# Optimization experiments

Measured on AMD Instinct MI355X. Metric: run time of the kernel, lower is better.

## Reference

```python
import jax, jax.numpy as jnp
import numpy as np

EPS = 1e-5
B, D_ENT, D_REL = 1024, 400, 400
OUT, KW = 32, 9
N_ENT = 50000


def _bn(x, g, b, axes):
    # batch-norm with batch statistics (training-mode math), eps=1e-5
    mu = jnp.mean(x, axis=axes, keepdims=True)
    var = jnp.var(x, axis=axes, keepdims=True)
    return (x - mu) * jax.lax.rsqrt(var + EPS) * g + b


def setup_inputs() -> dict:
    key = jax.random.key(0)
    ks = jax.random.split(key, 6)
    return {
        "e1_emb": jax.random.normal(ks[0], (B, D_ENT), jnp.float32),
        "rel_emb": jax.random.normal(ks[1], (B, D_REL), jnp.float32),
        "all_ent_w": jax.random.normal(ks[2], (N_ENT, D_ENT), jnp.float32),
        "fc1_w": jax.random.normal(ks[3], (OUT * KW, D_REL), jnp.float32) * 0.05,
        "fc1_b": jnp.zeros((OUT * KW,), jnp.float32),
        "fc_w": jax.random.normal(ks[4], (D_ENT, (D_ENT - KW + 1) * OUT), jnp.float32) * 0.02,
        "fc_b": jnp.zeros((D_ENT,), jnp.float32),
        "bn0_g": jnp.ones((1,), jnp.float32),
        "bn0_b": jnp.zeros((1,), jnp.float32),
        "bn1_g": jnp.ones((OUT,), jnp.float32),
        "bn1_b": jnp.zeros((OUT,), jnp.float32),
        "bn2_g": jnp.ones((D_ENT,), jnp.float32),
        "bn2_b": jnp.zeros((D_ENT,), jnp.float32),
    }


def reference(e1_emb, rel_emb, all_ent_w, fc1_w, fc1_b, fc_w, fc_b,
              bn0_g, bn0_b, bn1_g, bn1_b, bn2_g, bn2_b):
    d = e1_emb.shape[1]
    L = d - KW + 1  # conv output width (kernel_h=1, in_channels=1)

    # bn0: BatchNorm2d(1) over view [B,1,1,d] -> stats over all elements
    x = _bn(e1_emb, bn0_g, bn0_b, axes=(0, 1))  # [B, d]

    # hypernetwork: relation -> per-sample conv kernels [B, OUT, KW]
    k = (rel_emb @ fc1_w.T + fc1_b).reshape(-1, OUT, KW)

    # per-sample 1x9 conv (groups=B) as windows + batched contraction
    # xw[b, l, w] = x[b, l + w]
    xw = jnp.stack([x[:, w:w + L] for w in range(KW)], axis=-1)  # [B, L, KW]
    conv = jnp.einsum('blw,bow->bol', xw, k)  # [B, OUT, L]

    # bn1: BatchNorm2d(OUT), per-channel stats over (batch, width)
    h = _bn(conv, bn1_g[None, :, None], bn1_b[None, :, None], axes=(0, 2))

    # flatten channel-major (matches torch .view(B, -1) on [B, OUT, 1, L])
    h = h.reshape(h.shape[0], OUT * L)
    h = h @ fc_w.T + fc_b  # [B, d]

    # bn2: BatchNorm1d(d), per-feature stats over batch
    h = jax.nn.relu(_bn(h, bn2_g, bn2_b, axes=(0,)))

    return h @ all_ent_w.T  # [B, N_ENT]
```

## Files before the change

kernel.cpp:

```cpp
#include <hip/hip_runtime.h>
#include <stdint.h>

typedef unsigned short u16;
typedef short bf16x8 __attribute__((ext_vector_type(8)));
typedef float f32x4 __attribute__((ext_vector_type(4)));
typedef u16 u16x4 __attribute__((ext_vector_type(4)));
typedef u16 u16x8 __attribute__((ext_vector_type(8)));

#define B_SZ   1024
#define D_IN   400
#define L_OUT  392
#define OC     32
#define KW     9
#define K_FC   12544
#define N_ENT  50000
#define KPAD_H 448
#define NPAD_FC 512
#define SPLIT_FC 14

__device__ __forceinline__ u16 f2bf(float f) {
  uint32_t u = __builtin_bit_cast(uint32_t, f);
  u += 0x7FFFu + ((u >> 16) & 1u);
  return (u16)(u >> 16);
}
__device__ __forceinline__ float bf2f(u16 v) {
  uint32_t u = ((uint32_t)v) << 16;
  return __builtin_bit_cast(float, u);
}

__device__ __forceinline__ void gload_lds16(const u16* g, u16* l) {
  __builtin_amdgcn_global_load_lds(
      (const __attribute__((address_space(1))) unsigned int*)g,
      (__attribute__((address_space(3))) unsigned int*)l, 16, 0, 0);
}

__device__ __forceinline__ void block_reduce2(float& s1, float& s2, float* sm) {
  for (int d = 32; d; d >>= 1) { s1 += __shfl_down(s1, d); s2 += __shfl_down(s2, d); }
  int wave = threadIdx.x >> 6, lane = threadIdx.x & 63;
  if (lane == 0) { sm[wave * 2] = s1; sm[wave * 2 + 1] = s2; }
  __syncthreads();
  if (threadIdx.x == 0) {
    s1 = sm[0] + sm[2] + sm[4] + sm[6];
    s2 = sm[1] + sm[3] + sm[5] + sm[7];
  }
}

__global__ __launch_bounds__(256) void red0(const float* __restrict__ e1, float* __restrict__ part0) {
  int t = threadIdx.x;
  int idx = blockIdx.x * 256 + t;
  float s1 = 0.f, s2 = 0.f;
  for (int i = idx; i < B_SZ * D_IN; i += 256 * 256) { float v = e1[i]; s1 += v; s2 += v * v; }
  __shared__ float sm[8];
  block_reduce2(s1, s2, sm);
  if (t == 0) { part0[blockIdx.x * 2] = s1; part0[blockIdx.x * 2 + 1] = s2; }
}

__global__ __launch_bounds__(256) void fc1_gemm(const float* __restrict__ rel,
                                                const float* __restrict__ W,
                                                const float* __restrict__ bias,
                                                float* __restrict__ outk,
                                                const float* __restrict__ part0,
                                                const float* __restrict__ g0,
                                                const float* __restrict__ b0,
                                                float* __restrict__ stats) {
  __shared__ __align__(16) float As[16 * 68];
  __shared__ __align__(16) float Bs[16 * 68];
  __shared__ float sm0[8];
  int mt = blockIdx.x, nt = blockIdx.y;
  int t = threadIdx.x;
  int tx = t & 15, ty = t >> 4;
  int lr = t >> 2, lk = (t & 3) * 4;
  float acc[4][4] = {};
  for (int k0 = 0; k0 < 400; k0 += 16) {
    __syncthreads();
    float4 av = *(const float4*)(rel + (size_t)(mt * 64 + lr) * 400 + k0 + lk);
    int brow = nt * 64 + lr;
    float4 bv = {0.f, 0.f, 0.f, 0.f};
    if (brow < 288) bv = *(const float4*)(W + (size_t)brow * 400 + k0 + lk);
    As[(lk + 0) * 68 + lr] = av.x; As[(lk + 1) * 68 + lr] = av.y;
    As[(lk + 2) * 68 + lr] = av.z; As[(lk + 3) * 68 + lr] = av.w;
    Bs[(lk + 0) * 68 + lr] = bv.x; Bs[(lk + 1) * 68 + lr] = bv.y;
    Bs[(lk + 2) * 68 + lr] = bv.z; Bs[(lk + 3) * 68 + lr] = bv.w;
    __syncthreads();
#pragma unroll
    for (int k = 0; k < 16; ++k) {
      float4 a = *(const float4*)(As + k * 68 + ty * 4);
      float4 b = *(const float4*)(Bs + k * 68 + tx * 4);
      float aa[4] = {a.x, a.y, a.z, a.w}, bb[4] = {b.x, b.y, b.z, b.w};
#pragma unroll
      for (int i = 0; i < 4; ++i)
#pragma unroll
        for (int j = 0; j < 4; ++j) acc[i][j] += aa[i] * bb[j];
    }
  }
#pragma unroll
  for (int i = 0; i < 4; ++i) {
    int row = mt * 64 + ty * 4 + i;
#pragma unroll
    for (int j = 0; j < 4; ++j) {
      int col = nt * 64 + tx * 4 + j;
      if (col < 288) outk[(size_t)row * 288 + col] = acc[i][j] + bias[col];
    }
  }
  if (mt == 0 && nt == 0) {
    float s1 = part0[t * 2], s2 = part0[t * 2 + 1];
    __syncthreads();
    block_reduce2(s1, s2, sm0);
    if (t == 0) {
      const float N = (float)(B_SZ * D_IN);
      float mu = s1 / N, var = s2 / N - mu * mu;
      float a = g0[0] * rsqrtf(var + 1e-5f);
      stats[0] = a;
      stats[1] = b0[0] - mu * a;
    }
  }
}

__global__ __launch_bounds__(256) void conv_kernel(const float* __restrict__ e1,
                                                   const float* __restrict__ stats,
                                                   const float* __restrict__ kbuf,
                                                   u16* __restrict__ convA,
                                                   float* __restrict__ partial1) {
  int b = blockIdx.x, t = threadIdx.x;
  __shared__ __align__(16) float xs[D_IN];
  __shared__ float ks[OC * KW];
  float a0 = stats[0], b0c = stats[1];
  for (int i = t; i < D_IN; i += 256) xs[i] = e1[(size_t)b * D_IN + i] * a0 + b0c;
  for (int i = t; i < OC * KW; i += 256) ks[i] = kbuf[(size_t)b * (OC * KW) + i];
  __syncthreads();
  int o = t >> 3, sub = t & 7;
  float kw[KW];
#pragma unroll
  for (int w = 0; w < KW; ++w) kw[w] = ks[o * KW + w];
  float s1 = 0.f, s2 = 0.f;
  u16* orow = convA + (size_t)b * K_FC + o * L_OUT;
#pragma unroll
  for (int it = 0; it < 13; ++it) {
    int l = sub * 4 + it * 32;
    if (l < L_OUT) {
      float4 x0 = *(const float4*)(xs + l);
      float4 x1 = *(const float4*)(xs + l + 4);
      float4 x2 = *(const float4*)(xs + l + 8);
      float xv[12] = {x0.x, x0.y, x0.z, x0.w, x1.x, x1.y, x1.z, x1.w, x2.x, x2.y, x2.z, x2.w};
      u16x4 st;
#pragma unroll
      for (int j = 0; j < 4; ++j) {
        float c = 0.f;
#pragma unroll
        for (int w = 0; w < KW; ++w) c += xv[j + w] * kw[w];
        s1 += c; s2 += c * c;
        st[j] = f2bf(c);
      }
      *(u16x4*)(orow + l) = st;
    }
  }
  s1 += __shfl_down(s1, 4); s2 += __shfl_down(s2, 4);
  s1 += __shfl_down(s1, 2); s2 += __shfl_down(s2, 2);
  s1 += __shfl_down(s1, 1); s2 += __shfl_down(s2, 1);
  if (sub == 0) {
    partial1[b * 64 + o] = s1;
    partial1[b * 64 + 32 + o] = s2;
  }
}

__global__ __launch_bounds__(256) void comb1(const float* __restrict__ partial1,
                                             const float* __restrict__ g1,
                                             float* __restrict__ alphaK) {
  __shared__ float red[256];
  __shared__ float ab[32];
  int t = threadIdx.x;
  int s = t & 63, q = t >> 6;
  float acc = 0.f;
  for (int b = q * 256; b < q * 256 + 256; ++b) acc += partial1[b * 64 + s];
  red[t] = acc;
  __syncthreads();
  if (t < 64) red[t] = red[t] + red[t + 64] + red[t + 128] + red[t + 192];
  __syncthreads();
  if (t < 32) {
    const float N = (float)(B_SZ * L_OUT);
    float S1 = red[t], S2 = red[t + 32];
    float mu = S1 / N, var = S2 / N - mu * mu;
    ab[t] = g1[t] * rsqrtf(var + 1e-5f);
  }
  __syncthreads();
  for (int i = t; i < K_FC; i += 256) {
    int o = i / L_OUT;
    alphaK[i] = ab[o];
  }
}

__global__ __launch_bounds__(256) void cvt_fcw(const float* __restrict__ src,
                                               const float* __restrict__ alphaK,
                                               u16* __restrict__ dst) {
  int gid = blockIdx.x * 256 + threadIdx.x;
  int row = gid / 1568, c = gid - row * 1568;
  int k = c * 8;
  u16x8 o = {};
  if (row < 400) {
    float4 f0 = *(const float4*)(src + (size_t)row * K_FC + k);
    float4 f1 = *(const float4*)(src + (size_t)row * K_FC + k + 4);
    float4 a0 = *(const float4*)(alphaK + k);
    float4 a1 = *(const float4*)(alphaK + k + 4);
    o[0] = f2bf(f0.x * a0.x); o[1] = f2bf(f0.y * a0.y);
    o[2] = f2bf(f0.z * a0.z); o[3] = f2bf(f0.w * a0.w);
    o[4] = f2bf(f1.x * a1.x); o[5] = f2bf(f1.y * a1.y);
    o[6] = f2bf(f1.z * a1.z); o[7] = f2bf(f1.w * a1.w);
  }
  *(u16x8*)(dst + (size_t)row * K_FC + k) = o;
}

__global__ __launch_bounds__(256) void bn2_kernel(const float* __restrict__ part2,
                                                  const float* __restrict__ g2,
                                                  const float* __restrict__ b2,
                                                  u16* __restrict__ hfin) {
  int j0 = blockIdx.x * 16;
  int t = threadIdx.x;
  int tj = t & 15, tb = t >> 4;
  int j = j0 + tj;
  float v[64];
  float s1 = 0.f, s2 = 0.f;
#pragma unroll 2
  for (int i = 0; i < 64; ++i) {
    int b = tb + i * 16;
    float acc = 0.f;
#pragma unroll
    for (int s = 0; s < SPLIT_FC; ++s)
      acc += part2[((size_t)s * B_SZ + b) * NPAD_FC + j];
    v[i] = acc; s1 += acc; s2 += acc * acc;
  }
  __shared__ float sm1[16][17], sm2[16][17];
  sm1[tb][tj] = s1; sm2[tb][tj] = s2;
  __syncthreads();
  __shared__ float albe[2][16];
  if (t < 16) {
    float S1 = 0.f, S2 = 0.f;
#pragma unroll
    for (int r = 0; r < 16; ++r) { S1 += sm1[r][t]; S2 += sm2[r][t]; }
    int jf = j0 + t;
    float al = 0.f, be = 0.f;
    if (jf < D_IN) {
      float mu = S1 / 1024.f, var = S2 / 1024.f - mu * mu;
      al = g2[jf] * rsqrtf(var + 1e-5f);
      be = b2[jf] - mu * al;
    }
    albe[0][t] = al; albe[1][t] = be;
  }
  __syncthreads();
  float al = albe[0][tj], be = albe[1][tj];
#pragma unroll 2
  for (int i = 0; i < 64; ++i) {
    int b = tb + i * 16;
    hfin[(size_t)b * KPAD_H + j] = f2bf(fmaxf(v[i] * al + be, 0.f));
  }
}

__global__ __launch_bounds__(256) void gemm_bt(const u16* __restrict__ A,
                                               const u16* __restrict__ Bm,
                                               float* __restrict__ C,
                                               int Kpad, int mtiles, int ntiles,
                                               int ksteps_total, int ksteps_chunk,
                                               long ldc, int ncols_valid, long csplit_stride) {
  __shared__ __align__(16) u16 As[128 * 64];
  __shared__ __align__(16) u16 Bs[128 * 64];
  int bid = blockIdx.x;
  int mt = bid % mtiles;
  int nt = (bid / mtiles) % ntiles;
  int sp = bid / (mtiles * ntiles);
  int kbeg = sp * ksteps_chunk;
  int kend = kbeg + ksteps_chunk;
  if (kend > ksteps_total) kend = ksteps_total;

  int tid = threadIdx.x;
  int wave = tid >> 6, lane = tid & 63;
  int quad = lane >> 4, m16 = lane & 15;
  int rbase = (wave >> 1) * 64, cbase = (wave & 1) * 64;

  const u16* Arow0 = A + (size_t)mt * 128 * Kpad;
  const u16* Brow0 = Bm + (size_t)nt * 128 * Kpad;

  f32x4 acc[4][4] = {};

  for (int kt = kbeg; kt < kend; ++kt) {
    int k0 = kt * 64;
    __syncthreads();
#pragma unroll
    for (int p = 0; p < 4; ++p) {
      int slin = p * 256 + tid;
      int row = slin >> 3;
      int gch = (slin & 7) ^ (row & 7);
      u16* la = As + ((p * 256 + (wave << 6)) << 3);
      u16* lb = Bs + ((p * 256 + (wave << 6)) << 3);
      gload_lds16(Arow0 + (size_t)row * Kpad + k0 + gch * 8, la);
      gload_lds16(Brow0 + (size_t)row * Kpad + k0 + gch * 8, lb);
    }
    __syncthreads();
#pragma unroll
    for (int s = 0; s < 2; ++s) {
      bf16x8 af[4], bfr[4];
#pragma unroll
      for (int i = 0; i < 4; ++i) {
        int ar = rbase + i * 16 + m16;
        af[i] = *(const bf16x8*)(As + ar * 64 + (((s * 4 + quad) ^ (ar & 7)) << 3));
        int bc = cbase + i * 16 + m16;
        bfr[i] = *(const bf16x8*)(Bs + bc * 64 + (((s * 4 + quad) ^ (bc & 7)) << 3));
      }
#pragma unroll
      for (int i = 0; i < 4; ++i)
#pragma unroll
        for (int j = 0; j < 4; ++j)
          acc[i][j] = __builtin_amdgcn_mfma_f32_16x16x32_bf16(af[i], bfr[j], acc[i][j], 0, 0, 0);
    }
  }

  float* Cb = C + (size_t)sp * csplit_stride;
#pragma unroll
  for (int i = 0; i < 4; ++i) {
#pragma unroll
    for (int j = 0; j < 4; ++j) {
      int col = nt * 128 + cbase + j * 16 + m16;
      if (col < ncols_valid) {
        int row0 = mt * 128 + rbase + i * 16 + quad * 4;
#pragma unroll
        for (int r = 0; r < 4; ++r)
          Cb[(size_t)(row0 + r) * ldc + col] = acc[i][j][r];
      }
    }
  }
}

__global__ __launch_bounds__(256, 2) void gemm_ent(const u16* __restrict__ A,
                                                   const float* __restrict__ Bf,
                                                   float* __restrict__ C) {
  __shared__ __align__(16) u16 As[2][256 * 64];
  __shared__ __align__(16) u16 Bs[128 * 64];
  int bid = blockIdx.x;
  int r = bid & 7, g = bid >> 3;
  int mt = g & 3;
  int nt = (g >> 2) * 8 + r;
  if (nt >= 391) return;

  int tid = threadIdx.x;
  int wave = tid >> 6, lane = tid & 63;
  int quad = lane >> 4, m16 = lane & 15;
  int rbase = (wave >> 1) * 128, cbase = (wave & 1) * 64;

  const u16* Arow0 = A + (size_t)mt * 256 * KPAD_H;

  float4 fb[4][2];

#define LOAD_B(K0)                                                         \
  {                                                                        \
    _Pragma("unroll") for (int q = 0; q < 4; ++q) {                        \
      int slin = q * 256 + tid;                                            \
      int row = slin >> 3;                                                 \
      int gch = (slin & 7) ^ (row & 7);                                    \
      int gr = nt * 128 + row;                                             \
      int gk = (K0) + gch * 8;                                             \
      if (gr < N_ENT && gk < D_IN) {                                       \
        fb[q][0] = *(const float4*)(Bf + (size_t)gr * D_IN + gk);          \
        fb[q][1] = *(const float4*)(Bf + (size_t)gr * D_IN + gk + 4);      \
      } else {                                                             \
        fb[q][0] = float4{0.f, 0.f, 0.f, 0.f};                             \
        fb[q][1] = float4{0.f, 0.f, 0.f, 0.f};                             \
      }                                                                    \
    }                                                                      \
  }

#define STAGE_A(KT, BUF)                                                   \
  {                                                                        \
    _Pragma("unroll") for (int p = 0; p < 8; ++p) {                        \
      int slin = p * 256 + tid;                                            \
      int row = slin >> 3;                                                 \
      int gch = (slin & 7) ^ (row & 7);                                    \
      u16* la = As[BUF] + ((p * 256 + (wave << 6)) << 3);                  \
      gload_lds16(Arow0 + (size_t)row * KPAD_H + (KT) * 64 + gch * 8, la); \
    }                                                                      \
  }

#define WRITE_B()                                                          \
  {                                                                        \
    _Pragma("unroll") for (int q = 0; q < 4; ++q) {                        \
      int slin = q * 256 + tid;                                            \
      u16x8 st;                                                            \
      st[0] = f2bf(fb[q][0].x); st[1] = f2bf(fb[q][0].y);                  \
      st[2] = f2bf(fb[q][0].z); st[3] = f2bf(fb[q][0].w);                  \
      st[4] = f2bf(fb[q][1].x); st[5] = f2bf(fb[q][1].y);                  \
      st[6] = f2bf(fb[q][1].z); st[7] = f2bf(fb[q][1].w);                  \
      *(u16x8*)(Bs + slin * 8) = st;                                       \
    }                                                                      \
  }

  f32x4 acc[8][4] = {};

  LOAD_B(0)
  STAGE_A(0, 0)

#pragma unroll
  for (int kt = 0; kt < 7; ++kt) {
    int cur = kt & 1;
    WRITE_B()
    if (kt < 6) {
      LOAD_B((kt + 1) * 64)
      STAGE_A(kt + 1, cur ^ 1)
    }
    __builtin_amdgcn_sched_barrier(0);
    if (kt < 6) asm volatile("s_waitcnt vmcnt(16) lgkmcnt(0)" ::: "memory");
    else        asm volatile("s_waitcnt vmcnt(0) lgkmcnt(0)" ::: "memory");
    __builtin_amdgcn_sched_barrier(0);
    __builtin_amdgcn_s_barrier();
    __builtin_amdgcn_sched_barrier(0);

    __builtin_amdgcn_s_setprio(1);
#pragma unroll
    for (int s = 0; s < 2; ++s) {
      bf16x8 bfr[4];
#pragma unroll
      for (int j = 0; j < 4; ++j) {
        int bc = cbase + j * 16 + m16;
        bfr[j] = *(const bf16x8*)(Bs + bc * 64 + (((s * 4 + quad) ^ (bc & 7)) << 3));
      }
#pragma unroll
      for (int i = 0; i < 8; ++i) {
        int ar = rbase + i * 16 + m16;
        bf16x8 af = *(const bf16x8*)(As[cur] + ar * 64 + (((s * 4 + quad) ^ (ar & 7)) << 3));
#pragma unroll
        for (int j = 0; j < 4; ++j)
          acc[i][j] = __builtin_amdgcn_mfma_f32_16x16x32_bf16(af, bfr[j], acc[i][j], 0, 0, 0);
      }
    }
    __builtin_amdgcn_s_setprio(0);
    __builtin_amdgcn_sched_barrier(0);
    if (kt < 6) {
      __builtin_amdgcn_s_barrier();
      __builtin_amdgcn_sched_barrier(0);
    }
  }
#undef LOAD_B
#undef STAGE_A
#undef WRITE_B

#pragma unroll
  for (int i = 0; i < 8; ++i) {
#pragma unroll
    for (int j = 0; j < 4; ++j) {
      int col = nt * 128 + cbase + j * 16 + m16;
      if (col < N_ENT) {
        int row0 = mt * 256 + rbase + i * 16 + quad * 4;
#pragma unroll
        for (int rr = 0; rr < 4; ++rr)
          C[(size_t)(row0 + rr) * N_ENT + col] = acc[i][j][rr];
      }
    }
  }
}

extern "C" void kernel_launch(void* const* d_in, const int* in_sizes, int n_in,
                              void* d_out, int out_size, void* d_ws, size_t ws_size,
                              hipStream_t stream) {
  const float* e1   = (const float*)d_in[0];
  const float* rel  = (const float*)d_in[1];
  const float* entw = (const float*)d_in[2];
  const float* fc1w = (const float*)d_in[3];
  const float* fc1b = (const float*)d_in[4];
  const float* fcw  = (const float*)d_in[5];
  const float* bn0g = (const float*)d_in[7];
  const float* bn0b = (const float*)d_in[8];
  const float* bn1g = (const float*)d_in[9];
  const float* bn2g = (const float*)d_in[11];
  const float* bn2b = (const float*)d_in[12];
  float* out = (float*)d_out;

  char* ws = (char*)d_ws;
  size_t off = 0;
  auto alloc = [&](size_t bytes) -> void* {
    off = (off + 255) & ~(size_t)255;
    void* p = ws + off;
    off += bytes;
    return p;
  };
  float* stats    = (float*)alloc(16 * 4);
  float* part0    = (float*)alloc(512 * 4);
  float* kbuf     = (float*)alloc((size_t)B_SZ * 288 * 4);
  float* partial1 = (float*)alloc((size_t)B_SZ * 64 * 4);
  float* alphaK   = (float*)alloc((size_t)K_FC * 4);
  u16*   convA    = (u16*)alloc((size_t)B_SZ * K_FC * 2);
  u16*   fcwb     = (u16*)alloc((size_t)NPAD_FC * K_FC * 2);
  float* part2    = (float*)alloc((size_t)SPLIT_FC * B_SZ * NPAD_FC * 4);
  u16*   hfin     = (u16*)alloc((size_t)B_SZ * KPAD_H * 2);

  red0<<<256, 256, 0, stream>>>(e1, part0);
  fc1_gemm<<<dim3(16, 5), 256, 0, stream>>>(rel, fc1w, fc1b, kbuf, part0, bn0g, bn0b, stats);
  conv_kernel<<<B_SZ, 256, 0, stream>>>(e1, stats, kbuf, convA, partial1);
  comb1<<<1, 256, 0, stream>>>(partial1, bn1g, alphaK);
  cvt_fcw<<<3136, 256, 0, stream>>>(fcw, alphaK, fcwb);
  gemm_bt<<<8 * 4 * SPLIT_FC, 256, 0, stream>>>(convA, fcwb, part2, K_FC, 8, 4, 196, 14,
                                                (long)NPAD_FC, NPAD_FC, (long)B_SZ * NPAD_FC);
  bn2_kernel<<<KPAD_H / 16, 256, 0, stream>>>(part2, bn2g, bn2b, hfin);
  gemm_ent<<<8 * 4 * 49, 256, 0, stream>>>(hfin, entw, out);
}
```

Baseline: 551.1 us.

## Shrink gemm_ent tile to 128x128 and double-buffer B with deeper prefetch

Reduces the entity GEMM block tile from 256x128 to 128x128, which doubles the grid and halves the accumulators per wave. The B tile (fp32 entity weights converted to bf16) is now double-buffered in LDS and prefetched two k-steps ahead in registers. The conversion and LDS write are moved after the MFMA loop, so each iteration needs only one barrier. The intent is to hide global-load latency and raise occupancy. The cost is that the fp32 entity weights are reloaded twice as often, since there are 8 M-tiles instead of 4.

```diff
diff --git a/kernel.cpp b/kernel.cpp
--- a/kernel.cpp
+++ b/kernel.cpp
@@ -331,24 +331,24 @@
 __global__ __launch_bounds__(256, 2) void gemm_ent(const u16* __restrict__ A,
                                                    const float* __restrict__ Bf,
                                                    float* __restrict__ C) {
-  __shared__ __align__(16) u16 As[2][256 * 64];
-  __shared__ __align__(16) u16 Bs[128 * 64];
+  __shared__ __align__(16) u16 As[2][128 * 64];
+  __shared__ __align__(16) u16 Bs[2][128 * 64];
   int bid = blockIdx.x;
   int r = bid & 7, g = bid >> 3;
-  int mt = g & 3;
-  int nt = (g >> 2) * 8 + r;
+  int mt = g & 7;
+  int nt = (g >> 3) * 8 + r;
   if (nt >= 391) return;
 
   int tid = threadIdx.x;
   int wave = tid >> 6, lane = tid & 63;
   int quad = lane >> 4, m16 = lane & 15;
-  int rbase = (wave >> 1) * 128, cbase = (wave & 1) * 64;
-
-  const u16* Arow0 = A + (size_t)mt * 256 * KPAD_H;
-
-  float4 fb[4][2];
-
-#define LOAD_B(K0)                                                         \
+  int rbase = (wave >> 1) * 64, cbase = (wave & 1) * 64;
+
+  const u16* Arow0 = A + (size_t)mt * 128 * KPAD_H;
+
+  float4 fb[2][8];
+
+#define LOAD_B(K0, FB)                                                     \
   {                                                                        \
     _Pragma("unroll") for (int q = 0; q < 4; ++q) {                        \
       int slin = q * 256 + tid;                                            \
@@ -357,18 +357,18 @@
       int gr = nt * 128 + row;                                             \
       int gk = (K0) + gch * 8;                                             \
       if (gr < N_ENT && gk < D_IN) {                                       \
-        fb[q][0] = *(const float4*)(Bf + (size_t)gr * D_IN + gk);          \
-        fb[q][1] = *(const float4*)(Bf + (size_t)gr * D_IN + gk + 4);      \
+        fb[FB][q * 2]     = *(const float4*)(Bf + (size_t)gr * D_IN + gk); \
+        fb[FB][q * 2 + 1] = *(const float4*)(Bf + (size_t)gr * D_IN + gk + 4); \
       } else {                                                             \
-        fb[q][0] = float4{0.f, 0.f, 0.f, 0.f};                             \
-        fb[q][1] = float4{0.f, 0.f, 0.f, 0.f};                             \
+        fb[FB][q * 2]     = float4{0.f, 0.f, 0.f, 0.f};                    \
+        fb[FB][q * 2 + 1] = float4{0.f, 0.f, 0.f, 0.f};                    \
       }                                                                    \
     }                                                                      \
   }
 
 #define STAGE_A(KT, BUF)                                                   \
   {                                                                        \
-    _Pragma("unroll") for (int p = 0; p < 8; ++p) {                        \
+    _Pragma("unroll") for (int p = 0; p < 4; ++p) {                        \
       int slin = p * 256 + tid;                                            \
       int row = slin >> 3;                                                 \
       int gch = (slin & 7) ^ (row & 7);                                    \
@@ -377,60 +377,69 @@
     }                                                                      \
   }
 
-#define WRITE_B()                                                          \
+#define WRITE_B(FB, BUF)                                                   \
   {                                                                        \
     _Pragma("unroll") for (int q = 0; q < 4; ++q) {                        \
       int slin = q * 256 + tid;                                            \
       u16x8 st;                                                            \
-      st[0] = f2bf(fb[q][0].x); st[1] = f2bf(fb[q][0].y);                  \
-      st[2] = f2bf(fb[q][0].z); st[3] = f2bf(fb[q][0].w);                  \
-      st[4] = f2bf(fb[q][1].x); st[5] = f2bf(fb[q][1].y);                  \
-      st[6] = f2bf(fb[q][1].z); st[7] = f2bf(fb[q][1].w);                  \
-      *(u16x8*)(Bs + slin * 8) = st;                                       \
+      st[0] = f2bf(fb[FB][q * 2].x);     st[1] = f2bf(fb[FB][q * 2].y);    \
+      st[2] = f2bf(fb[FB][q * 2].z);     st[3] = f2bf(fb[FB][q * 2].w);    \
+      st[4] = f2bf(fb[FB][q * 2 + 1].x); st[5] = f2bf(fb[FB][q * 2 + 1].y);\
+      st[6] = f2bf(fb[FB][q * 2 + 1].z); st[7] = f2bf(fb[FB][q * 2 + 1].w);\
+      *(u16x8*)(Bs[BUF] + slin * 8) = st;                                  \
     }                                                                      \
   }
 
-  f32x4 acc[8][4] = {};
-
-  LOAD_B(0)
+  f32x4 acc[4][4] = {};
+
+  LOAD_B(0, 0)
   STAGE_A(0, 0)
-
-#pragma unroll
-  for (int kt = 0; kt < 7; ++kt) {
-    int cur = kt & 1;
-    WRITE_B()
-    if (kt < 6) {
-      LOAD_B((kt + 1) * 64)
-      STAGE_A(kt + 1, cur ^ 1)
-    }
+  LOAD_B(64, 1)
+  __builtin_amdgcn_sched_barrier(0);
+  asm volatile("s_waitcnt vmcnt(8)");
+  __builtin_amdgcn_sched_barrier(0);
+  WRITE_B(0, 0)
+  __builtin_amdgcn_sched_barrier(0);
+  asm volatile("s_waitcnt lgkmcnt(0)");
+  __builtin_amdgcn_sched_barrier(0);
+  __builtin_amdgcn_s_barrier();
+  __builtin_amdgcn_sched_barrier(0);
+
+#pragma unroll
+  for (int t = 0; t < 7; ++t) {
+    const int cur = t & 1;
+    if (t < 6) STAGE_A(t + 1, cur ^ 1)
+    if (t < 5) LOAD_B((t + 2) * 64, t & 1)
     __builtin_amdgcn_sched_barrier(0);
-    if (kt < 6) asm volatile("s_waitcnt vmcnt(16) lgkmcnt(0)" ::: "memory");
-    else        asm volatile("s_waitcnt vmcnt(0) lgkmcnt(0)" ::: "memory");
-    __builtin_amdgcn_sched_barrier(0);
-    __builtin_amdgcn_s_barrier();
-    __builtin_amdgcn_sched_barrier(0);
 
     __builtin_amdgcn_s_setprio(1);
 #pragma unroll
     for (int s = 0; s < 2; ++s) {
-      bf16x8 bfr[4];
-#pragma unroll
-      for (int j = 0; j < 4; ++j) {
-        int bc = cbase + j * 16 + m16;
-        bfr[j] = *(const bf16x8*)(Bs + bc * 64 + (((s * 4 + quad) ^ (bc & 7)) << 3));
+      bf16x8 af[4], bfr[4];
+#pragma unroll
+      for (int i = 0; i < 4; ++i) {
+        int ar = rbase + i * 16 + m16;
+        af[i] = *(const bf16x8*)(As[cur] + ar * 64 + (((s * 4 + quad) ^ (ar & 7)) << 3));
+        int bc = cbase + i * 16 + m16;
+        bfr[i] = *(const bf16x8*)(Bs[cur] + bc * 64 + (((s * 4 + quad) ^ (bc & 7)) << 3));
       }
 #pragma unroll
-      for (int i = 0; i < 8; ++i) {
-        int ar = rbase + i * 16 + m16;
-        bf16x8 af = *(const bf16x8*)(As[cur] + ar * 64 + (((s * 4 + quad) ^ (ar & 7)) << 3));
+      for (int i = 0; i < 4; ++i)
 #pragma unroll
         for (int j = 0; j < 4; ++j)
-          acc[i][j] = __builtin_amdgcn_mfma_f32_16x16x32_bf16(af, bfr[j], acc[i][j], 0, 0, 0);
-      }
+          acc[i][j] = __builtin_amdgcn_mfma_f32_16x16x32_bf16(af[i], bfr[j], acc[i][j], 0, 0, 0);
     }
     __builtin_amdgcn_s_setprio(0);
     __builtin_amdgcn_sched_barrier(0);
-    if (kt < 6) {
+
+    if (t < 6) {
+      if (t < 5) asm volatile("s_waitcnt vmcnt(8)");
+      else       asm volatile("s_waitcnt vmcnt(0)");
+      __builtin_amdgcn_sched_barrier(0);
+      WRITE_B((t + 1) & 1, cur ^ 1)
+      __builtin_amdgcn_sched_barrier(0);
+      asm volatile("s_waitcnt lgkmcnt(0)");
+      __builtin_amdgcn_sched_barrier(0);
       __builtin_amdgcn_s_barrier();
       __builtin_amdgcn_sched_barrier(0);
     }
@@ -440,12 +449,12 @@
 #undef WRITE_B
 
 #pragma unroll
-  for (int i = 0; i < 8; ++i) {
+  for (int i = 0; i < 4; ++i) {
 #pragma unroll
     for (int j = 0; j < 4; ++j) {
       int col = nt * 128 + cbase + j * 16 + m16;
       if (col < N_ENT) {
-        int row0 = mt * 256 + rbase + i * 16 + quad * 4;
+        int row0 = mt * 128 + rbase + i * 16 + quad * 4;
 #pragma unroll
         for (int rr = 0; rr < 4; ++rr)
           C[(size_t)(row0 + rr) * N_ENT + col] = acc[i][j][rr];
@@ -496,5 +505,5 @@
   gemm_bt<<<8 * 4 * SPLIT_FC, 256, 0, stream>>>(convA, fcwb, part2, K_FC, 8, 4, 196, 14,
                                                 (long)NPAD_FC, NPAD_FC, (long)B_SZ * NPAD_FC);
   bn2_kernel<<<KPAD_H / 16, 256, 0, stream>>>(part2, bn2g, bn2b, hfin);
-  gemm_ent<<<8 * 4 * 49, 256, 0, stream>>>(hfin, entw, out);
-}
+  gemm_ent<<<8 * 392, 256, 0, stream>>>(hfin, entw, out);
+}
```

After: 573.3 us. 1.04x slower.
